# Kernel tuning notes

Hardware: AMD Instinct MI355X
Metric: run time of the kernel (lower is better)

## Reference

```python
import jax, jax.numpy as jnp
import numpy as np

ALPHA = 1.5  # entmax alpha (EntmaxBisect default behavior, exponent 1/(alpha-1)=2)
N_ITER = 50  # EntmaxBisect default number of bisection iterations


def entmax_bisect(x, alpha=ALPHA, n_iter=N_ITER):
    """Entmax via bisection along the last axis (Peters & Martins), matching
    the torch entmax.EntmaxBisect forward (with ensure_sum_one=True)."""
    d = x.shape[-1]
    xs = x * (alpha - 1.0)
    max_val = jnp.max(xs, axis=-1, keepdims=True)
    tau_lo = max_val - 1.0
    tau_hi = max_val - (1.0 / d) ** (alpha - 1.0)

    inv_am1 = 1.0 / (alpha - 1.0)  # = 2.0 for alpha=1.5

    def p(tau):
        return jnp.maximum(xs - tau, 0.0) ** inv_am1

    f_lo = jnp.sum(p(tau_lo), axis=-1, keepdims=True) - 1.0
    dm0 = tau_hi - tau_lo

    def body(i, carry):
        tau_lo, dm = carry
        dm = dm * 0.5
        tau_m = tau_lo + dm
        f_m = jnp.sum(p(tau_m), axis=-1, keepdims=True) - 1.0
        tau_lo = jnp.where(f_m * f_lo >= 0, tau_m, tau_lo)
        return (tau_lo, dm)

    tau_lo, dm = jax.lax.fori_loop(0, n_iter, body, (tau_lo, dm0))
    p_m = p(tau_lo + dm)
    return p_m / jnp.sum(p_m, axis=-1, keepdims=True)


def setup_inputs() -> dict:
    key = jax.random.key(0)
    k1, k2, k3, k4 = jax.random.split(key, 4)
    bsz, nfield, nemb = 2048, 128, 128
    nhead, nhid, d_k = 8, 64, 64

    def xavier(k, shape, gain=1.414):
        fan_in, fan_out = shape[-2], shape[-1]
        std = gain * np.sqrt(2.0 / (fan_in + fan_out))
        return jax.random.normal(k, shape, dtype=jnp.float32) * std

    return {
        "x": jax.random.normal(k1, (bsz, nfield, nemb), dtype=jnp.float32),
        "bilinear_w": xavier(k2, (nhead, nemb, d_k)),
        "query": xavier(k3, (nhead, nhid, d_k)),
        "values": xavier(k4, (nhead, nhid, nfield)),
    }


def reference(x, bilinear_w, query, values):
    # x: [b, f, x(=nemb)]; bilinear_w: [k, x, y(=d_k)]; query: [k, o(=nhid), y]
    d_k = bilinear_w.shape[-1]
    scale = d_k ** (-0.5)
    # einsum('bfx,kxy,koy->bkof') split into two contractions
    kx = jnp.einsum('bfx,kxy->bkfy', x, bilinear_w)            # [b,k,f,y]
    att_gates = jnp.einsum('bkfy,koy->bkof', kx, query) * scale  # [b,k,o,f]
    sparse_gates = entmax_bisect(att_gates)
    return sparse_gates * values[None]  # einsum('bkof,kof->bkof')
```

## Files before the change

kernel.cpp:

```cpp
#include <hip/hip_runtime.h>
#include <hip/hip_bf16.h>


using half8_t  = __attribute__((ext_vector_type(8))) _Float16;
using half4_t  = __attribute__((ext_vector_type(4))) _Float16;
using floatx4  = __attribute__((ext_vector_type(4))) float;

#define NITER 18

__global__ __launch_bounds__(256) void w2_kernel(const float* __restrict__ bw,
                                                 const float* __restrict__ qm,
                                                 _Float16* __restrict__ W2h) {
    const int k  = blockIdx.x >> 3;
    const int og = blockIdx.x & 7;
    __shared__ float Lbw[128 * 65];
    __shared__ float Lq[8 * 64];
    const int t = threadIdx.x;

    const float* bwk = bw + k * 8192;
    #pragma unroll
    for (int i2 = 0; i2 < 8; ++i2) {
        int i = t + i2 * 256;
        float4 v = ((const float4*)bwk)[i];
        int xx = (i * 4) >> 6, y = (i * 4) & 63;
        float* dst = &Lbw[xx * 65 + y];
        dst[0] = v.x; dst[1] = v.y; dst[2] = v.z; dst[3] = v.w;
    }
    const float* qk = qm + k * 4096 + og * 8 * 64;
    if (t < 128) ((float4*)Lq)[t] = ((const float4*)qk)[t];
    __syncthreads();

    #pragma unroll
    for (int i = 0; i < 4; ++i) {
        int ox = i * 256 + t;
        int o = ox >> 7, x = ox & 127;
        const float* brow = &Lbw[x * 65];
        const float* qrow = &Lq[o * 64];
        float acc = 0.f;
        #pragma unroll
        for (int y = 0; y < 64; ++y) acc = fmaf(brow[y], qrow[y], acc);
        W2h[(k * 64 + og * 8 + o) * 128 + x] = (_Float16)(acc * 0.0625f);
    }
}

__global__ __launch_bounds__(256, 3) void satt_kernel(
        const float* __restrict__ xg, const _Float16* __restrict__ W2h,
        const float* __restrict__ values, float* __restrict__ out) {
    const int bid = blockIdx.x;
    const int b = bid >> 3, k = bid & 7;
    const int t = threadIdx.x;
    const int w = t >> 6, l = t & 63;

    __shared__ __align__(16) char smem[52224];
    _Float16* Ash = (_Float16*)smem;
    _Float16* Bsh = (_Float16*)(smem + 17408);
    float*    zsh = (float*)smem;

    const _Float16* w2k = W2h + k * 8192;
    #pragma unroll
    for (int j = 0; j < 4; ++j) {
        int c = t + 256 * j;
        int o = c >> 4, x0 = (c & 15) * 8;
        uint4 v = ((const uint4*)w2k)[c];
        *(uint4*)(Ash + o * 136 + x0) = v;
    }
    const float* xb = xg + (size_t)b * 16384;
    #pragma unroll
    for (int j = 0; j < 16; ++j) {
        int c = t + 256 * j;
        int f = c >> 5, x0 = (c & 31) * 4;
        float4 v = ((const float4*)xb)[c];
        half4_t h;
        h[0] = (_Float16)v.x; h[1] = (_Float16)v.y;
        h[2] = (_Float16)v.z; h[3] = (_Float16)v.w;
        *(half4_t*)(Bsh + f * 136 + x0) = h;
    }
    __syncthreads();

    const int q = l >> 4, c16 = l & 15;
    half8_t afrag[4];
    #pragma unroll
    for (int kk = 0; kk < 4; ++kk)
        afrag[kk] = *(const half8_t*)(Ash + (w * 16 + c16) * 136 + kk * 32 + q * 8);

    floatx4 acc[8];
    #pragma unroll
    for (int ft = 0; ft < 8; ++ft) acc[ft] = (floatx4){0.f, 0.f, 0.f, 0.f};

    #pragma unroll
    for (int kk = 0; kk < 4; ++kk) {
        #pragma unroll
        for (int ft = 0; ft < 8; ++ft) {
            half8_t bfrag = *(const half8_t*)(Bsh + (ft * 16 + c16) * 136 + kk * 32 + q * 8);
            acc[ft] = __builtin_amdgcn_mfma_f32_16x16x32_f16(afrag[kk], bfrag, acc[ft], 0, 0, 0);
        }
    }
    __syncthreads();

    #pragma unroll
    for (int ft = 0; ft < 8; ++ft) {
        #pragma unroll
        for (int r = 0; r < 4; ++r)
            zsh[(w * 16 + q * 4 + r) * 132 + ft * 16 + c16] = acc[ft][r];
    }
    __syncthreads();

    const int row = l >> 2, s = l & 3;
    const int o = w * 16 + row;
    float zz[32];
    #pragma unroll
    for (int j = 0; j < 8; ++j) {
        floatx4 v = *(const floatx4*)(zsh + o * 132 + s * 32 + j * 4);
        zz[4 * j + 0] = v[0]; zz[4 * j + 1] = v[1];
        zz[4 * j + 2] = v[2]; zz[4 * j + 3] = v[3];
    }
    float m = zz[0];
    #pragma unroll
    for (int j = 1; j < 32; ++j) m = fmaxf(m, zz[j]);
    m = fmaxf(m, __shfl_xor(m, 1));
    m = fmaxf(m, __shfl_xor(m, 2));

    float tau = m - 1.0f;
    float dm  = 0.9116116523516816f;
    float ssum = 0.f;
    #pragma unroll
    for (int j = 0; j < 32; ++j) { float d = fmaxf(zz[j] - tau, 0.f); ssum = fmaf(d, d, ssum); }
    ssum += __shfl_xor(ssum, 1); ssum += __shfl_xor(ssum, 2);
    const float f_lo = ssum - 1.0f;

    for (int it = 0; it < NITER; ++it) {
        dm *= 0.5f;
        float tm = tau + dm;
        float sa = 0.f;
        #pragma unroll
        for (int j = 0; j < 32; ++j) { float d = fmaxf(zz[j] - tm, 0.f); sa = fmaf(d, d, sa); }
        sa += __shfl_xor(sa, 1); sa += __shfl_xor(sa, 2);
        float fm = sa - 1.0f;
        tau = (fm * f_lo >= 0.f) ? tm : tau;
    }
    const float te = tau + dm;
    float ps = 0.f;
    #pragma unroll
    for (int j = 0; j < 32; ++j) {
        float d = fmaxf(zz[j] - te, 0.f);
        float p = d * d;
        zz[j] = p;
        ps += p;
    }
    ps += __shfl_xor(ps, 1); ps += __shfl_xor(ps, 2);
    const float inv = 1.0f / ps;

    const float* vrow = values + ((k * 64 + o) * 128 + s * 32);
    float* orow = out + ((((size_t)b * 8 + k) * 64 + o) * 128 + s * 32);
    #pragma unroll
    for (int j = 0; j < 8; ++j) {
        floatx4 vv = *(const floatx4*)(vrow + 4 * j);
        floatx4 g;
        g[0] = zz[4 * j + 0] * inv * vv[0];
        g[1] = zz[4 * j + 1] * inv * vv[1];
        g[2] = zz[4 * j + 2] * inv * vv[2];
        g[3] = zz[4 * j + 3] * inv * vv[3];
        *(floatx4*)(orow + 4 * j) = g;
    }
}

extern "C" void kernel_launch(void* const* d_in, const int* in_sizes, int n_in,
                              void* d_out, int out_size, void* d_ws, size_t ws_size,
                              hipStream_t stream) {
    const float* xg     = (const float*)d_in[0];
    const float* bw     = (const float*)d_in[1];
    const float* qm     = (const float*)d_in[2];
    const float* values = (const float*)d_in[3];
    float* out = (float*)d_out;
    _Float16* W2h = (_Float16*)d_ws;

    w2_kernel<<<64, 256, 0, stream>>>(bw, qm, W2h);
    satt_kernel<<<16384, 256, 0, stream>>>(xg, W2h, values, out);
}
```

Baseline: 827.8 us.

## Replace bisection with fp16 coarse bisection plus Newton refinement for entmax threshold

Cuts the entmax threshold search from 18 fp32 bisection steps to 8 packed-fp16 bisection steps using fdot2, followed by two fp16 and one fp32 Newton steps on the quadratic sum. It also drops the f_lo evaluation by comparing the sum directly against 1, and remaps block indices so that blocks sharing a head are scheduled together. This reduces per-row ALU work in the dominant loop. The cost is reduced precision in the coarse fp16 phase, and Newton convergence is assumed to reach the reference result.

```diff
diff --git a/kernel.cpp b/kernel.cpp
--- a/kernel.cpp
+++ b/kernel.cpp
@@ -4,9 +4,27 @@
 
 using half8_t  = __attribute__((ext_vector_type(8))) _Float16;
 using half4_t  = __attribute__((ext_vector_type(4))) _Float16;
+using fp16x2   = __attribute__((ext_vector_type(2))) __fp16;
 using floatx4  = __attribute__((ext_vector_type(4))) float;
 
-#define NITER 18
+#define NBIS 8
+
+#if defined(__has_builtin)
+#if __has_builtin(__builtin_amdgcn_fdot2)
+#define HAS_FDOT2 1
+#endif
+#endif
+#ifndef HAS_FDOT2
+#define HAS_FDOT2 0
+#endif
+
+__device__ __forceinline__ float frcp(float x) {
+#if __has_builtin(__builtin_amdgcn_rcpf)
+    return __builtin_amdgcn_rcpf(x);
+#else
+    return 1.0f / x;
+#endif
+}
 
 __global__ __launch_bounds__(256) void w2_kernel(const float* __restrict__ bw,
                                                  const float* __restrict__ qm,
@@ -47,7 +65,8 @@
         const float* __restrict__ xg, const _Float16* __restrict__ W2h,
         const float* __restrict__ values, float* __restrict__ out) {
     const int bid = blockIdx.x;
-    const int b = bid >> 3, k = bid & 7;
+    const int k = (bid & 511) >> 6;
+    const int b = ((bid >> 9) << 6) | (bid & 63);
     const int t = threadIdx.x;
     const int w = t >> 6, l = t & 63;
 
@@ -114,39 +133,118 @@
         zz[4 * j + 0] = v[0]; zz[4 * j + 1] = v[1];
         zz[4 * j + 2] = v[2]; zz[4 * j + 3] = v[3];
     }
-    float m = zz[0];
-    #pragma unroll
-    for (int j = 1; j < 32; ++j) m = fmaxf(m, zz[j]);
+    float m0 = zz[0], m1 = zz[1], m2 = zz[2], m3 = zz[3];
+    #pragma unroll
+    for (int j = 4; j < 32; j += 4) {
+        m0 = fmaxf(m0, zz[j + 0]); m1 = fmaxf(m1, zz[j + 1]);
+        m2 = fmaxf(m2, zz[j + 2]); m3 = fmaxf(m3, zz[j + 3]);
+    }
+    float m = fmaxf(fmaxf(m0, m1), fmaxf(m2, m3));
     m = fmaxf(m, __shfl_xor(m, 1));
     m = fmaxf(m, __shfl_xor(m, 2));
 
     float tau = m - 1.0f;
     float dm  = 0.9116116523516816f;
-    float ssum = 0.f;
-    #pragma unroll
-    for (int j = 0; j < 32; ++j) { float d = fmaxf(zz[j] - tau, 0.f); ssum = fmaf(d, d, ssum); }
-    ssum += __shfl_xor(ssum, 1); ssum += __shfl_xor(ssum, 2);
-    const float f_lo = ssum - 1.0f;
-
-    for (int it = 0; it < NITER; ++it) {
+
+#if HAS_FDOT2
+    fp16x2 zh[16];
+    #pragma unroll
+    for (int j = 0; j < 16; ++j)
+        zh[j] = __builtin_amdgcn_cvt_pkrtz(zz[2 * j], zz[2 * j + 1]);
+    const fp16x2 hzero = { (__fp16)0.f, (__fp16)0.f };
+    const fp16x2 hone  = { (__fp16)1.f, (__fp16)1.f };
+
+    #pragma unroll
+    for (int it = 0; it < NBIS; ++it) {
         dm *= 0.5f;
         float tm = tau + dm;
-        float sa = 0.f;
-        #pragma unroll
-        for (int j = 0; j < 32; ++j) { float d = fmaxf(zz[j] - tm, 0.f); sa = fmaf(d, d, sa); }
-        sa += __shfl_xor(sa, 1); sa += __shfl_xor(sa, 2);
-        float fm = sa - 1.0f;
-        tau = (fm * f_lo >= 0.f) ? tm : tau;
-    }
-    const float te = tau + dm;
-    float ps = 0.f;
-    #pragma unroll
-    for (int j = 0; j < 32; ++j) {
-        float d = fmaxf(zz[j] - te, 0.f);
-        float p = d * d;
-        zz[j] = p;
-        ps += p;
-    }
+        fp16x2 t2 = __builtin_amdgcn_cvt_pkrtz(tm, tm);
+        float sa = 0.f, sb = 0.f;
+        #pragma unroll
+        for (int j = 0; j < 16; j += 2) {
+            fp16x2 d0 = __builtin_elementwise_max(zh[j]     - t2, hzero);
+            fp16x2 d1 = __builtin_elementwise_max(zh[j + 1] - t2, hzero);
+            sa = __builtin_amdgcn_fdot2(d0, d0, sa, false);
+            sb = __builtin_amdgcn_fdot2(d1, d1, sb, false);
+        }
+        float sm = sa + sb;
+        sm += __shfl_xor(sm, 1); sm += __shfl_xor(sm, 2);
+        tau = (sm >= 1.0f) ? tm : tau;
+    }
+    #pragma unroll
+    for (int it = 0; it < 2; ++it) {
+        fp16x2 t2 = __builtin_amdgcn_cvt_pkrtz(tau, tau);
+        float s2a = 0.f, s2b = 0.f, s1a = 0.f, s1b = 0.f;
+        #pragma unroll
+        for (int j = 0; j < 16; j += 2) {
+            fp16x2 d0 = __builtin_elementwise_max(zh[j]     - t2, hzero);
+            fp16x2 d1 = __builtin_elementwise_max(zh[j + 1] - t2, hzero);
+            s2a = __builtin_amdgcn_fdot2(d0, d0, s2a, false);
+            s2b = __builtin_amdgcn_fdot2(d1, d1, s2b, false);
+            s1a = __builtin_amdgcn_fdot2(d0, hone, s1a, false);
+            s1b = __builtin_amdgcn_fdot2(d1, hone, s1b, false);
+        }
+        float s2 = s2a + s2b, s1 = s1a + s1b;
+        s2 += __shfl_xor(s2, 1); s2 += __shfl_xor(s2, 2);
+        s1 += __shfl_xor(s1, 1); s1 += __shfl_xor(s1, 2);
+        tau += (s2 - 1.0f) * frcp(fmaxf(s1 + s1, 1e-6f));
+    }
+#else
+    #pragma unroll
+    for (int it = 0; it < NBIS + 4; ++it) {
+        dm *= 0.5f;
+        float tm = tau + dm;
+        float sa = 0.f, sb = 0.f;
+        #pragma unroll
+        for (int j = 0; j < 32; j += 2) {
+            float d0 = fmaxf(zz[j] - tm, 0.f);
+            float d1 = fmaxf(zz[j + 1] - tm, 0.f);
+            sa = fmaf(d0, d0, sa); sb = fmaf(d1, d1, sb);
+        }
+        float sm = sa + sb;
+        sm += __shfl_xor(sm, 1); sm += __shfl_xor(sm, 2);
+        tau = (sm >= 1.0f) ? tm : tau;
+    }
+    {
+        float s2a = 0.f, s2b = 0.f, s1a = 0.f, s1b = 0.f;
+        #pragma unroll
+        for (int j = 0; j < 32; j += 2) {
+            float d0 = fmaxf(zz[j] - tau, 0.f);
+            float d1 = fmaxf(zz[j + 1] - tau, 0.f);
+            s2a = fmaf(d0, d0, s2a); s2b = fmaf(d1, d1, s2b);
+            s1a += d0; s1b += d1;
+        }
+        float s2 = s2a + s2b, s1 = s1a + s1b;
+        s2 += __shfl_xor(s2, 1); s2 += __shfl_xor(s2, 2);
+        s1 += __shfl_xor(s1, 1); s1 += __shfl_xor(s1, 2);
+        tau += (s2 - 1.0f) * frcp(fmaxf(s1 + s1, 1e-6f));
+    }
+#endif
+    {
+        float s2a = 0.f, s2b = 0.f, s1a = 0.f, s1b = 0.f;
+        #pragma unroll
+        for (int j = 0; j < 32; j += 2) {
+            float d0 = fmaxf(zz[j] - tau, 0.f);
+            float d1 = fmaxf(zz[j + 1] - tau, 0.f);
+            s2a = fmaf(d0, d0, s2a); s2b = fmaf(d1, d1, s2b);
+            s1a += d0; s1b += d1;
+        }
+        float s2 = s2a + s2b, s1 = s1a + s1b;
+        s2 += __shfl_xor(s2, 1); s2 += __shfl_xor(s2, 2);
+        s1 += __shfl_xor(s1, 1); s1 += __shfl_xor(s1, 2);
+        tau += (s2 - 1.0f) * frcp(fmaxf(s1 + s1, 1e-6f));
+    }
+
+    float ps0 = 0.f, ps1 = 0.f;
+    #pragma unroll
+    for (int j = 0; j < 32; j += 2) {
+        float d0 = fmaxf(zz[j] - tau, 0.f);
+        float d1 = fmaxf(zz[j + 1] - tau, 0.f);
+        float p0 = d0 * d0, p1 = d1 * d1;
+        zz[j] = p0; zz[j + 1] = p1;
+        ps0 += p0; ps1 += p1;
+    }
+    float ps = ps0 + ps1;
     ps += __shfl_xor(ps, 1); ps += __shfl_xor(ps, 2);
     const float inv = 1.0f / ps;
 
```

After: 816.4 us. Within noise of the previous version (-1.4%).
